# Kernel tuning notes

Hardware: AMD Instinct MI355X
Metric: run time of the kernel (lower is better)

## Reference

```python
import jax, jax.numpy as jnp
import numpy as np

B, N, D_IN = 2, 2048, 2048
D_OUT, H, KV = 2048, 32, 8
G = H // KV          # group_size = 4
DH = D_OUT // H      # head dim = 64


def setup_inputs() -> dict:
    key = jax.random.key(0)
    k0, k1, k2, k3, k4, k5 = jax.random.split(key, 6)
    s_in = 1.0 / np.sqrt(D_IN)
    s_out = 1.0 / np.sqrt(D_OUT)
    return {
        "x": jax.random.normal(k0, (B, N, D_IN), dtype=jnp.float32),
        "Wq": jax.random.normal(k1, (D_IN, H * DH), dtype=jnp.float32) * s_in,
        "Wk": jax.random.normal(k2, (D_IN, KV * DH), dtype=jnp.float32) * s_in,
        "Wv": jax.random.normal(k3, (D_IN, KV * DH), dtype=jnp.float32) * s_in,
        "Wo": jax.random.normal(k4, (D_OUT, D_IN), dtype=jnp.float32) * s_out,
        "bo": jax.random.normal(k5, (D_IN,), dtype=jnp.float32) * 0.01,
    }


def gqa_forward(x, Wq, Wk, Wv, Wo, bo):
    b, n, _ = x.shape
    scale = 1.0 / jnp.sqrt(jnp.asarray(DH, x.dtype))
    # projections
    q = (x @ Wq).reshape(b, n, KV, G, DH)   # queries grouped by shared kv head
    k = (x @ Wk).reshape(b, n, KV, DH)
    v = (x @ Wv).reshape(b, n, KV, DH)
    # scores: (B, KV, G, N, N) — equivalent to repeat_interleave of K over groups
    scores = jnp.einsum('bnkgd,bmkd->bkgnm', q, k) * scale
    causal = jnp.triu(jnp.ones((n, n), dtype=bool), k=1)
    scores = jnp.where(causal, -jnp.inf, scores)
    attn = jax.nn.softmax(scores, axis=-1)
    # dropout p=0.0 -> identity
    ctx = jnp.einsum('bkgnm,bmkd->bnkgd', attn, v).reshape(b, n, D_OUT)
    return ctx @ Wo + bo


def reference(x, Wq, Wk, Wv, Wo, bo):
    return gqa_forward(x, Wq, Wk, Wv, Wo, bo)
```

## Files before the change

kernel.cpp:

```cpp
#include <hip/hip_runtime.h>
#include <hip/hip_bf16.h>
#include <cstdint>


#define B_    2
#define N_    2048
#define DIN_  2048
#define H_    32
#define KV_   8
#define DH_   64
#define M_    4096
#define NQKV_ 3072

typedef float f32x4 __attribute__((ext_vector_type(4)));
typedef __bf16 bf16x8 __attribute__((ext_vector_type(8)));
typedef unsigned short u16x8 __attribute__((ext_vector_type(8)));

__device__ __forceinline__ unsigned short f32_to_bf16_bits(float f) {
  unsigned int u = __float_as_uint(f);
  u = (u + 0x7FFFu + ((u >> 16) & 1u)) >> 16;
  return (unsigned short)u;
}

__device__ __forceinline__ void gload_lds16(const void* g, void* l) {
  __builtin_amdgcn_global_load_lds(
      (__attribute__((address_space(1))) void*)(g),
      (__attribute__((address_space(3))) void*)(l), 16, 0, 0);
}

__global__ __launch_bounds__(256) void prep(
    const float* __restrict__ x, const float* __restrict__ Wq,
    const float* __restrict__ Wk, const float* __restrict__ Wv,
    const float* __restrict__ Wo,
    unsigned short* __restrict__ Xb, unsigned short* __restrict__ Wqkv,
    unsigned short* __restrict__ Wot, float qscale) {
  const int task = blockIdx.y, tid = threadIdx.x;
  if (task == 0) {
    size_t i0 = ((size_t)blockIdx.x * 256 + tid) * 2;
#pragma unroll
    for (int t = 0; t < 2; ++t) {
      float4 v = ((const float4*)x)[i0 + t];
      ushort4 o;
      o.x = f32_to_bf16_bits(v.x);
      o.y = f32_to_bf16_bits(v.y);
      o.z = f32_to_bf16_bits(v.z);
      o.w = f32_to_bf16_bits(v.w);
      ((ushort4*)Xb)[i0 + t] = o;
    }
    return;
  }
  const float* src;
  unsigned short* dst;
  int NC, off;
  float scale = 1.0f;
  switch (task) {
    case 1: src = Wq; dst = Wqkv; NC = 2048; off = 0;    scale = qscale; break;
    case 2: src = Wk; dst = Wqkv; NC = 512;  off = 2048; break;
    case 3: src = Wv; dst = Wqkv; NC = 512;  off = 2560; break;
    default: src = Wo; dst = Wot; NC = 2048; off = 0;    break;
  }
  const int nx = NC >> 5;
  const int bx = blockIdx.x;
  if (bx >= nx * 64) return;
  const int n0 = (bx % nx) * 32, k0 = (bx / nx) * 32;
  __shared__ float tile[32][33];
  const int tx = tid & 31, ty = tid >> 5;
#pragma unroll
  for (int i = 0; i < 32; i += 8)
    tile[ty + i][tx] = src[(size_t)(k0 + ty + i) * NC + n0 + tx];
  __syncthreads();
#pragma unroll
  for (int i = 0; i < 32; i += 8)
    dst[(size_t)(off + n0 + ty + i) * 2048 + k0 + tx] =
        f32_to_bf16_bits(tile[tx][ty + i] * scale);
}

__global__ __launch_bounds__(256) void transpose_v(
    const unsigned short* __restrict__ QKV, unsigned short* __restrict__ Vtg) {
  __shared__ unsigned short t[64][72];
  int nt = blockIdx.x, bkv = blockIdx.y;
  int b = bkv >> 3, kv = bkv & 7;
  int tid = threadIdx.x;
  int row = tid >> 2, c = (tid & 3) * 16;
  const unsigned short* src =
      QKV + (size_t)(b * N_ + nt * 64 + row) * NQKV_ + 2560 + kv * 64;
  *(u16x8*)&t[row][c]     = *(const u16x8*)(src + c);
  *(u16x8*)&t[row][c + 8] = *(const u16x8*)(src + c + 8);
  __syncthreads();
  int d = tid >> 2;
  unsigned short* dst = Vtg + ((size_t)bkv * 64 + d) * N_ + nt * 64 + c;
  u16x8 o0, o1;
#pragma unroll
  for (int i = 0; i < 8; ++i) { o0[i] = t[c + i][d]; o1[i] = t[c + 8 + i][d]; }
  *(u16x8*)dst = o0;
  *(u16x8*)(dst + 8) = o1;
}

template <bool OUT_BF16, bool BIAS>
__global__ __launch_bounds__(256, 3) void gemm_bt(
    const unsigned short* __restrict__ A,
    const unsigned short* __restrict__ Bt,
    void* __restrict__ Cv,
    const float* __restrict__ bias,
    int Nn, int K) {
  __shared__ unsigned short As[128 * 32];
  __shared__ unsigned short Bs[128 * 32];

  const int tid = threadIdx.x;
  const int lane = tid & 63;
  const int wave = tid >> 6;
  const int wm = wave >> 1, wn = wave & 1;
  const int l16 = lane & 15, quad = lane >> 4;
  const int m0 = blockIdx.y * 128, n0 = blockIdx.x * 128;

  f32x4 acc[4][4] = {};

  const int srow = tid >> 2;
  const int kc = tid & 3;

  for (int kk = 0; kk < K; kk += 32) {
#pragma unroll
    for (int c = 0; c < 2; ++c) {
      int r = c * 64 + srow;
      int ofs = r * 32 + kc * 8;
      gload_lds16(A + (size_t)(m0 + r) * K + kk + kc * 8, (char*)As + ofs * 2);
      gload_lds16(Bt + (size_t)(n0 + r) * K + kk + kc * 8, (char*)Bs + ofs * 2);
    }
    __syncthreads();
    bf16x8 af[4], bfr[4];
#pragma unroll
    for (int mi = 0; mi < 4; ++mi)
      af[mi] = *(const bf16x8*)&As[(wm * 64 + mi * 16 + l16) * 32 + quad * 8];
#pragma unroll
    for (int ni = 0; ni < 4; ++ni)
      bfr[ni] = *(const bf16x8*)&Bs[(wn * 64 + ni * 16 + l16) * 32 + quad * 8];
#pragma unroll
    for (int mi = 0; mi < 4; ++mi)
#pragma unroll
      for (int ni = 0; ni < 4; ++ni)
        acc[mi][ni] = __builtin_amdgcn_mfma_f32_16x16x32_bf16(
            af[mi], bfr[ni], acc[mi][ni], 0, 0, 0);
    __syncthreads();
  }

  unsigned short* Cb = (unsigned short*)Cv;
  float* Cf = (float*)Cv;
#pragma unroll
  for (int mi = 0; mi < 4; ++mi) {
    int rrow = m0 + wm * 64 + mi * 16 + quad * 4;
#pragma unroll
    for (int ni = 0; ni < 4; ++ni) {
      int col = n0 + wn * 64 + ni * 16 + l16;
      float bv = BIAS ? bias[col] : 0.0f;
#pragma unroll
      for (int r = 0; r < 4; ++r) {
        float v = acc[mi][ni][r] + bv;
        if (OUT_BF16)
          Cb[(size_t)(rrow + r) * Nn + col] = f32_to_bf16_bits(v);
        else
          Cf[(size_t)(rrow + r) * Nn + col] = v;
      }
    }
  }
}

__global__ __launch_bounds__(256, 2) void attn_fwd(
    const unsigned short* __restrict__ QKV,
    const unsigned short* __restrict__ Vtg,
    unsigned short* __restrict__ Ctx) {
  __shared__ unsigned short Ks[2][64 * 64];
  __shared__ unsigned short Vs[2][64 * 64];
  __shared__ unsigned short Ps[2][4][2][16 * 64];

  const int p = blockIdx.x;
  const int kv = blockIdx.y >> 1, hp = blockIdx.y & 1;
  const int b = blockIdx.z;
  const int tid = threadIdx.x, lane = tid & 63, wave = tid >> 6;
  const int l16 = lane & 15, quad = lane >> 4;
  const int h = kv * 4 + hp * 2 + (wave >> 1);
  const int rhalf = (wave & 1) * 32;
  const size_t baserow = (size_t)b * N_;
  const unsigned short* Kg = QKV + 2048 + kv * 64;
  const unsigned short* Vg = Vtg + (size_t)(b * KV_ + kv) * 64 * N_;
  const unsigned short* Qbase = QKV + baserow * NQKV_ + h * 64;
  const int sw = l16 & 7;

  auto stageKV = [&](int j, int buf) {
#pragma unroll
    for (int it = 0; it < 2; ++it) {
      int c = tid + it * 256;
      int row = c >> 3, off = ((c & 7) ^ (row & 7)) * 8;
      gload_lds16(Kg + (baserow + j * 64 + row) * NQKV_ + off,
                  (char*)Ks[buf] + c * 16);
      gload_lds16(Vg + (size_t)row * N_ + j * 64 + off,
                  (char*)Vs[buf] + c * 16);
    }
  };

#pragma unroll 1
  for (int phase = 0; phase < 2; ++phase) {
    const int qtile = phase ? p : 31 - p;
    const int q0 = qtile * 64;

    bf16x8 qa[2][2];
#pragma unroll
    for (int s = 0; s < 2; ++s)
#pragma unroll
      for (int ks = 0; ks < 2; ++ks)
        qa[s][ks] = *(const bf16x8*)(Qbase +
            (size_t)(q0 + rhalf + s * 16 + l16) * NQKV_ + ks * 32 + quad * 8);

    f32x4 oacc[2][4] = {};
    float lp[2][4] = {};

    __syncthreads();
    stageKV(0, 0);

    for (int j = 0; j <= qtile; ++j) {
      __syncthreads();
      const int buf = j & 1;
      if (j < qtile) stageKV(j + 1, buf ^ 1);

      bf16x8 kb[2][4];
#pragma unroll
      for (int ks = 0; ks < 2; ++ks)
#pragma unroll
        for (int ni = 0; ni < 4; ++ni)
          kb[ks][ni] = *(const bf16x8*)&Ks[buf][(ni * 16 + l16) * 64 +
                                               ((ks * 4 + quad) ^ sw) * 8];

#pragma unroll
      for (int s = 0; s < 2; ++s) {
        f32x4 sc[4] = {};
        __builtin_amdgcn_s_setprio(1);
#pragma unroll
        for (int ks = 0; ks < 2; ++ks)
#pragma unroll
          for (int ni = 0; ni < 4; ++ni)
            sc[ni] = __builtin_amdgcn_mfma_f32_16x16x32_bf16(
                qa[s][ks], kb[ks][ni], sc[ni], 0, 0, 0);
        __builtin_amdgcn_s_setprio(0);
        if (j == qtile) {
          const int qrow = q0 + rhalf + s * 16 + quad * 4;
#pragma unroll
          for (int ni = 0; ni < 4; ++ni) {
            int kcol = q0 + ni * 16 + l16;
#pragma unroll
            for (int r = 0; r < 4; ++r)
              if (kcol > qrow + r) sc[ni][r] = -1e30f;
          }
        }
        unsigned short* Pw = &Ps[buf][wave][s][0];
#pragma unroll
        for (int ni = 0; ni < 4; ++ni) {
          const int cl = ni * 2 + (l16 >> 3);
#pragma unroll
          for (int r = 0; r < 4; ++r) {
            float pe = __builtin_amdgcn_exp2f(sc[ni][r]);
            lp[s][r] += pe;
            int row = quad * 4 + r;
            Pw[row * 64 + ((cl ^ (row & 7)) * 8) + (l16 & 7)] =
                (unsigned short)(__float_as_uint(pe) >> 16);
          }
        }
      }

      bf16x8 vb[2][4];
#pragma unroll
      for (int ks = 0; ks < 2; ++ks)
#pragma unroll
        for (int di = 0; di < 4; ++di)
          vb[ks][di] = *(const bf16x8*)&Vs[buf][(di * 16 + l16) * 64 +
                                               ((ks * 4 + quad) ^ sw) * 8];
#pragma unroll
      for (int s = 0; s < 2; ++s) {
        bf16x8 pa[2];
#pragma unroll
        for (int ks = 0; ks < 2; ++ks)
          pa[ks] = *(const bf16x8*)&Ps[buf][wave][s][l16 * 64 +
                                                    ((ks * 4 + quad) ^ sw) * 8];
        __builtin_amdgcn_s_setprio(1);
#pragma unroll
        for (int ks = 0; ks < 2; ++ks)
#pragma unroll
          for (int di = 0; di < 4; ++di)
            oacc[s][di] = __builtin_amdgcn_mfma_f32_16x16x32_bf16(
                pa[ks], vb[ks][di], oacc[s][di], 0, 0, 0);
        __builtin_amdgcn_s_setprio(0);
      }
    }

#pragma unroll
    for (int s = 0; s < 2; ++s) {
      float inv[4];
#pragma unroll
      for (int r = 0; r < 4; ++r) {
        float v = lp[s][r];
#pragma unroll
        for (int off = 1; off < 16; off <<= 1) v += __shfl_xor(v, off);
        inv[r] = 1.0f / v;
      }
#pragma unroll
      for (int di = 0; di < 4; ++di)
#pragma unroll
        for (int r = 0; r < 4; ++r) {
          size_t row = baserow + q0 + rhalf + s * 16 + quad * 4 + r;
          Ctx[row * 2048 + h * 64 + di * 16 + l16] =
              f32_to_bf16_bits(oacc[s][di][r] * inv[r]);
        }
    }
  }
}

extern "C" void kernel_launch(void* const* d_in, const int* in_sizes, int n_in,
                              void* d_out, int out_size, void* d_ws, size_t ws_size,
                              hipStream_t stream) {
  const float* x  = (const float*)d_in[0];
  const float* Wq = (const float*)d_in[1];
  const float* Wk = (const float*)d_in[2];
  const float* Wv = (const float*)d_in[3];
  const float* Wo = (const float*)d_in[4];
  const float* bo = (const float*)d_in[5];
  float* out = (float*)d_out;

  unsigned short* Xb   = (unsigned short*)d_ws;
  unsigned short* Wqkv = Xb + (size_t)M_ * DIN_;
  unsigned short* QKV  = Wqkv + (size_t)NQKV_ * DIN_;
  unsigned short* Wot  = QKV + (size_t)M_ * NQKV_;
  unsigned short* Ctx  = Xb;
  unsigned short* Vtg  = Wqkv;

  const float kQScale = 0.125f * 1.44269504088896340736f;

  prep<<<dim3(4096, 5), 256, 0, stream>>>(x, Wq, Wk, Wv, Wo, Xb, Wqkv, Wot, kQScale);

  gemm_bt<true, false><<<dim3(NQKV_ / 128, M_ / 128), 256, 0, stream>>>(
      Xb, Wqkv, QKV, nullptr, NQKV_, DIN_);

  transpose_v<<<dim3(N_ / 64, B_ * KV_), 256, 0, stream>>>(QKV, Vtg);

  attn_fwd<<<dim3(16, 16, 2), 256, 0, stream>>>(QKV, Vtg, Ctx);

  gemm_bt<false, true><<<dim3(DIN_ / 128, M_ / 128), 256, 0, stream>>>(
      Ctx, Wot, out, bo, DIN_, 2048);
}
```

Baseline: 292.4 us.

## Rewrite GEMM as 256x256 tile with 4-stage LDS pipeline and swizzle

Replaces the 128x128 single-buffered GEMM with a 512-thread kernel that computes 256x256 tiles. It uses a 4-deep ring of LDS buffers with explicit vmcnt waits, an XOR-swizzled LDS layout to avoid bank conflicts, split A-half loads interleaved with MFMA, s_setprio around MFMA bursts, and a block-ID remap for L2 locality. The aim is to overlap global loads with compute and raise data reuse per tile. In exchange it launches far fewer workgroups (192 and 128 on a machine with 256 CUs), which risks leaving CUs idle, and it uses more registers.

```diff
diff --git a/kernel.cpp b/kernel.cpp
--- a/kernel.cpp
+++ b/kernel.cpp
@@ -97,57 +97,109 @@
 }
 
 template <bool OUT_BF16, bool BIAS>
-__global__ __launch_bounds__(256, 3) void gemm_bt(
+__global__ __launch_bounds__(512, 2) void gemm256(
     const unsigned short* __restrict__ A,
     const unsigned short* __restrict__ Bt,
     void* __restrict__ Cv,
     const float* __restrict__ bias,
-    int Nn, int K) {
-  __shared__ unsigned short As[128 * 32];
-  __shared__ unsigned short Bs[128 * 32];
+    int Nn, int K, int nbx) {
+  __shared__ unsigned short lds[4][2][8192];
 
   const int tid = threadIdx.x;
   const int lane = tid & 63;
   const int wave = tid >> 6;
-  const int wm = wave >> 1, wn = wave & 1;
+  const int wm = wave >> 2, wn = wave & 3;
   const int l16 = lane & 15, quad = lane >> 4;
-  const int m0 = blockIdx.y * 128, n0 = blockIdx.x * 128;
-
-  f32x4 acc[4][4] = {};
-
-  const int srow = tid >> 2;
-  const int kc = tid & 3;
-
-  for (int kk = 0; kk < K; kk += 32) {
+
+  const int nwg = gridDim.x;
+  const int orig = blockIdx.x;
+  const int bid = (orig & 7) * (nwg >> 3) + (orig >> 3);
+  const int m0 = (bid / nbx) * 256, n0 = (bid % nbx) * 256;
+
+  const int T = K >> 5;
+
+  auto stage = [&](int t, int part, const unsigned short* src, int r0) {
+    unsigned short* db = &lds[t & 3][part][0];
 #pragma unroll
     for (int c = 0; c < 2; ++c) {
-      int r = c * 64 + srow;
-      int ofs = r * 32 + kc * 8;
-      gload_lds16(A + (size_t)(m0 + r) * K + kk + kc * 8, (char*)As + ofs * 2);
-      gload_lds16(Bt + (size_t)(n0 + r) * K + kk + kc * 8, (char*)Bs + ofs * 2);
-    }
-    __syncthreads();
-    bf16x8 af[4], bfr[4];
-#pragma unroll
-    for (int mi = 0; mi < 4; ++mi)
-      af[mi] = *(const bf16x8*)&As[(wm * 64 + mi * 16 + l16) * 32 + quad * 8];
-#pragma unroll
-    for (int ni = 0; ni < 4; ++ni)
-      bfr[ni] = *(const bf16x8*)&Bs[(wn * 64 + ni * 16 + l16) * 32 + quad * 8];
+      int off = c * 8192 + tid * 16;
+      int row = off >> 6;
+      int kch = ((off >> 4) & 3) ^ ((row >> 1) & 3);
+      gload_lds16(src + (size_t)(r0 + row) * K + t * 32 + kch * 8,
+                  (char*)db + off);
+    }
+  };
+
+  f32x4 acc[8][4] = {};
+
+#pragma unroll
+  for (int t = 0; t < 3; ++t) {
+    stage(t, 0, A, m0);
+    stage(t, 1, Bt, n0);
+  }
+
+  for (int t = 0; t < T; ++t) {
+    if (t + 2 < T)      asm volatile("s_waitcnt vmcnt(8)" ::: "memory");
+    else if (t + 1 < T) asm volatile("s_waitcnt vmcnt(4)" ::: "memory");
+    else                asm volatile("s_waitcnt vmcnt(0)" ::: "memory");
+    __builtin_amdgcn_s_barrier();
+    asm volatile("" ::: "memory");
+
+    const char* Ab = (const char*)&lds[t & 3][0][0];
+    const char* Bb = (const char*)&lds[t & 3][1][0];
+
+    bf16x8 a[4], b[4];
+#pragma unroll
+    for (int mi = 0; mi < 4; ++mi) {
+      int row = wm * 128 + mi * 16 + l16;
+      a[mi] = *(const bf16x8*)(Ab + row * 64 + (quad ^ ((row >> 1) & 3)) * 16);
+    }
+#pragma unroll
+    for (int ni = 0; ni < 4; ++ni) {
+      int row = wn * 64 + ni * 16 + l16;
+      b[ni] = *(const bf16x8*)(Bb + row * 64 + (quad ^ ((row >> 1) & 3)) * 16);
+    }
+    if (t + 3 < T) stage(t + 3, 0, A, m0);
+    asm volatile("" ::: "memory");
+    __builtin_amdgcn_s_barrier();
+    asm volatile("s_waitcnt lgkmcnt(0)" ::: "memory");
+    __builtin_amdgcn_s_setprio(1);
 #pragma unroll
     for (int mi = 0; mi < 4; ++mi)
 #pragma unroll
       for (int ni = 0; ni < 4; ++ni)
         acc[mi][ni] = __builtin_amdgcn_mfma_f32_16x16x32_bf16(
-            af[mi], bfr[ni], acc[mi][ni], 0, 0, 0);
-    __syncthreads();
+            a[mi], b[ni], acc[mi][ni], 0, 0, 0);
+    __builtin_amdgcn_s_setprio(0);
+    asm volatile("" ::: "memory");
+    __builtin_amdgcn_s_barrier();
+    asm volatile("" ::: "memory");
+
+    bf16x8 a2[4];
+#pragma unroll
+    for (int mi = 0; mi < 4; ++mi) {
+      int row = wm * 128 + 64 + mi * 16 + l16;
+      a2[mi] = *(const bf16x8*)(Ab + row * 64 + (quad ^ ((row >> 1) & 3)) * 16);
+    }
+    if (t + 3 < T) stage(t + 3, 1, Bt, n0);
+    asm volatile("" ::: "memory");
+    __builtin_amdgcn_s_barrier();
+    asm volatile("s_waitcnt lgkmcnt(0)" ::: "memory");
+    __builtin_amdgcn_s_setprio(1);
+#pragma unroll
+    for (int mi = 0; mi < 4; ++mi)
+#pragma unroll
+      for (int ni = 0; ni < 4; ++ni)
+        acc[mi + 4][ni] = __builtin_amdgcn_mfma_f32_16x16x32_bf16(
+            a2[mi], b[ni], acc[mi + 4][ni], 0, 0, 0);
+    __builtin_amdgcn_s_setprio(0);
   }
 
   unsigned short* Cb = (unsigned short*)Cv;
   float* Cf = (float*)Cv;
 #pragma unroll
-  for (int mi = 0; mi < 4; ++mi) {
-    int rrow = m0 + wm * 64 + mi * 16 + quad * 4;
+  for (int mi = 0; mi < 8; ++mi) {
+    int rrow = m0 + wm * 128 + mi * 16 + quad * 4;
 #pragma unroll
     for (int ni = 0; ni < 4; ++ni) {
       int col = n0 + wn * 64 + ni * 16 + l16;
@@ -334,13 +386,13 @@
 
   prep<<<dim3(4096, 5), 256, 0, stream>>>(x, Wq, Wk, Wv, Wo, Xb, Wqkv, Wot, kQScale);
 
-  gemm_bt<true, false><<<dim3(NQKV_ / 128, M_ / 128), 256, 0, stream>>>(
-      Xb, Wqkv, QKV, nullptr, NQKV_, DIN_);
+  gemm256<true, false><<<dim3(192), 512, 0, stream>>>(
+      Xb, Wqkv, QKV, nullptr, NQKV_, DIN_, NQKV_ / 256);
 
   transpose_v<<<dim3(N_ / 64, B_ * KV_), 256, 0, stream>>>(QKV, Vtg);
 
   attn_fwd<<<dim3(16, 16, 2), 256, 0, stream>>>(QKV, Vtg, Ctx);
 
-  gemm_bt<false, true><<<dim3(DIN_ / 128, M_ / 128), 256, 0, stream>>>(
-      Ctx, Wot, out, bo, DIN_, 2048);
-}
+  gemm256<false, true><<<dim3(128), 512, 0, stream>>>(
+      Ctx, Wot, out, bo, DIN_, 2048, DIN_ / 256);
+}
```

Result: slower. 303.5 us (+3.8%).

## Pipeline GEMM with 4-stage LDS ring, swizzled layout and XCD-aware block remap

Applied to the files above, without the earlier changes.

Replaces the single-buffered bf16 GEMM with a 4-slot LDS ring buffer. Global-to-LDS loads are issued three k-steps ahead and gated by vmcnt waits with a single barrier per step, and register fragments are double-buffered so MFMA work overlaps the next LDS reads. The LDS layout gets an XOR swizzle to avoid bank conflicts, and the grid is flattened and remapped so consecutive tiles are spread across the 8 XCDs. MFMA sections also raise wave priority. LDS use grows to 64 KB per block and occupancy drops to 2 blocks per CU.

```diff
diff --git a/kernel.cpp b/kernel.cpp
--- a/kernel.cpp
+++ b/kernel.cpp
@@ -97,50 +97,94 @@
 }
 
 template <bool OUT_BF16, bool BIAS>
-__global__ __launch_bounds__(256, 3) void gemm_bt(
+__global__ __launch_bounds__(256, 2) void gemm128p(
     const unsigned short* __restrict__ A,
     const unsigned short* __restrict__ Bt,
     void* __restrict__ Cv,
     const float* __restrict__ bias,
-    int Nn, int K) {
-  __shared__ unsigned short As[128 * 32];
-  __shared__ unsigned short Bs[128 * 32];
+    int Nn, int K, int nbx) {
+  __shared__ unsigned short lds[4][2][4096];
 
   const int tid = threadIdx.x;
   const int lane = tid & 63;
   const int wave = tid >> 6;
   const int wm = wave >> 1, wn = wave & 1;
   const int l16 = lane & 15, quad = lane >> 4;
-  const int m0 = blockIdx.y * 128, n0 = blockIdx.x * 128;
+
+  const int nwg = gridDim.x;
+  const int orig = blockIdx.x;
+  const int bid = (orig & 7) * (nwg >> 3) + (orig >> 3);
+  const int m0 = (bid / nbx) * 128, n0 = (bid % nbx) * 128;
+
+  const int T = K >> 5;
+
+  auto stage = [&](int t) {
+    const int slot = t & 3;
+#pragma unroll
+    for (int c = 0; c < 2; ++c) {
+      int off = c * 4096 + tid * 16;
+      int row = off >> 6;
+      int kch = ((off >> 4) & 3) ^ ((row >> 1) & 3);
+      gload_lds16(A + (size_t)(m0 + row) * K + t * 32 + kch * 8,
+                  (char*)&lds[slot][0][0] + off);
+      gload_lds16(Bt + (size_t)(n0 + row) * K + t * 32 + kch * 8,
+                  (char*)&lds[slot][1][0] + off);
+    }
+  };
+
+  const int swz = (quad ^ ((l16 >> 1) & 3)) * 16;
+  const int rdA = (wm * 64 + l16) * 64 + swz;
+  const int rdB = (wn * 64 + l16) * 64 + swz;
+
+  auto rdfrags = [&](int tt, bf16x8 (&fa)[4], bf16x8 (&fb)[4]) {
+    const char* Ab = (const char*)&lds[tt & 3][0][0];
+    const char* Bb = (const char*)&lds[tt & 3][1][0];
+#pragma unroll
+    for (int mi = 0; mi < 4; ++mi)
+      fa[mi] = *(const bf16x8*)(Ab + rdA + mi * 1024);
+#pragma unroll
+    for (int ni = 0; ni < 4; ++ni)
+      fb[ni] = *(const bf16x8*)(Bb + rdB + ni * 1024);
+  };
 
   f32x4 acc[4][4] = {};
 
-  const int srow = tid >> 2;
-  const int kc = tid & 3;
-
-  for (int kk = 0; kk < K; kk += 32) {
-#pragma unroll
-    for (int c = 0; c < 2; ++c) {
-      int r = c * 64 + srow;
-      int ofs = r * 32 + kc * 8;
-      gload_lds16(A + (size_t)(m0 + r) * K + kk + kc * 8, (char*)As + ofs * 2);
-      gload_lds16(Bt + (size_t)(n0 + r) * K + kk + kc * 8, (char*)Bs + ofs * 2);
-    }
-    __syncthreads();
-    bf16x8 af[4], bfr[4];
-#pragma unroll
-    for (int mi = 0; mi < 4; ++mi)
-      af[mi] = *(const bf16x8*)&As[(wm * 64 + mi * 16 + l16) * 32 + quad * 8];
-#pragma unroll
-    for (int ni = 0; ni < 4; ++ni)
-      bfr[ni] = *(const bf16x8*)&Bs[(wn * 64 + ni * 16 + l16) * 32 + quad * 8];
+  auto domfma = [&](bf16x8 (&fa)[4], bf16x8 (&fb)[4]) {
+    __builtin_amdgcn_s_setprio(1);
 #pragma unroll
     for (int mi = 0; mi < 4; ++mi)
 #pragma unroll
       for (int ni = 0; ni < 4; ++ni)
         acc[mi][ni] = __builtin_amdgcn_mfma_f32_16x16x32_bf16(
-            af[mi], bfr[ni], acc[mi][ni], 0, 0, 0);
-    __syncthreads();
+            fa[mi], fb[ni], acc[mi][ni], 0, 0, 0);
+    __builtin_amdgcn_s_setprio(0);
+  };
+
+  auto gate = [&](int t) {
+    if (t + 2 < T)      asm volatile("s_waitcnt vmcnt(4)" ::: "memory");
+    else if (t + 1 < T) asm volatile("s_waitcnt vmcnt(0)" ::: "memory");
+    __builtin_amdgcn_s_barrier();
+    asm volatile("" ::: "memory");
+    if (t + 3 < T) stage(t + 3);
+  };
+
+  bf16x8 Aa[4], Ab_[4], Ba[4], Bb_[4];
+
+  stage(0); stage(1); stage(2);
+  asm volatile("s_waitcnt vmcnt(8)" ::: "memory");
+  __builtin_amdgcn_s_barrier();
+  asm volatile("" ::: "memory");
+  rdfrags(0, Aa, Ba);
+
+  for (int t = 0; t < T; t += 2) {
+    gate(t);
+    rdfrags(t + 1, Ab_, Bb_);
+    __builtin_amdgcn_sched_barrier(0);
+    domfma(Aa, Ba);
+    gate(t + 1);
+    if (t + 2 < T) rdfrags(t + 2, Aa, Ba);
+    __builtin_amdgcn_sched_barrier(0);
+    domfma(Ab_, Bb_);
   }
 
   unsigned short* Cb = (unsigned short*)Cv;
@@ -334,13 +378,13 @@
 
   prep<<<dim3(4096, 5), 256, 0, stream>>>(x, Wq, Wk, Wv, Wo, Xb, Wqkv, Wot, kQScale);
 
-  gemm_bt<true, false><<<dim3(NQKV_ / 128, M_ / 128), 256, 0, stream>>>(
-      Xb, Wqkv, QKV, nullptr, NQKV_, DIN_);
+  gemm128p<true, false><<<dim3(768), 256, 0, stream>>>(
+      Xb, Wqkv, QKV, nullptr, NQKV_, DIN_, NQKV_ / 128);
 
   transpose_v<<<dim3(N_ / 64, B_ * KV_), 256, 0, stream>>>(QKV, Vtg);
 
   attn_fwd<<<dim3(16, 16, 2), 256, 0, stream>>>(QKV, Vtg, Ctx);
 
-  gemm_bt<false, true><<<dim3(DIN_ / 128, M_ / 128), 256, 0, stream>>>(
-      Ctx, Wot, out, bo, DIN_, 2048);
-}
+  gemm128p<false, true><<<dim3(512), 256, 0, stream>>>(
+      Ctx, Wot, out, bo, DIN_, 2048, DIN_ / 128);
+}
```

Measured after the change: 288.0 us. About the same (-1.5%).
